# Kernel tuning notes

Measured on AMD Instinct MI355X. Metric: run time of the kernel, lower is better.

## Reference

```python
import jax, jax.numpy as jnp
import numpy as np

B, N, D, H = 8, 2048, 128, 4
DH = D // H
EPS_LN = 1e-5


def setup_inputs() -> dict:
    key = jax.random.key(0)
    ks = jax.random.split(key, 9)
    x = jax.random.normal(ks[0], (B, N, D), dtype=jnp.float32)
    u = jax.random.uniform(ks[1], (N, N), dtype=jnp.float32)
    adj = jnp.where(u > 0.5, u, 0.0)
    adj = adj.at[jnp.arange(N), jnp.arange(N)].set(1.0)
    W = jax.random.normal(ks[2], (D, D), dtype=jnp.float32) * (1.0 / np.sqrt(D))
    a_src = jax.random.normal(ks[3], (H, DH), dtype=jnp.float32) * 0.02
    a_dst = jax.random.normal(ks[4], (H, DH), dtype=jnp.float32) * 0.02
    Wo = jax.random.normal(ks[5], (D, D), dtype=jnp.float32) * (1.0 / np.sqrt(D))
    bo = jnp.zeros((D,), dtype=jnp.float32)
    gamma = jnp.ones((D,), dtype=jnp.float32)
    beta = jnp.zeros((D,), dtype=jnp.float32)
    return {"x": x, "adj_static": adj, "W": W, "a_src": a_src, "a_dst": a_dst,
            "Wo": Wo, "bo": bo, "gamma": gamma, "beta": beta}


def reference(x, adj_static, W, a_src, a_dst, Wo, bo, gamma, beta):
    # h: (B, H, N, DH)
    h = (x @ W.T).reshape(B, N, H, DH).transpose(0, 2, 1, 3)
    src = jnp.einsum('bhnd,hd->bhn', h, a_src)  # (B, H, N)
    dst = jnp.einsum('bhnd,hd->bhn', h, a_dst)  # (B, H, N)
    e = jax.nn.leaky_relu(src[..., :, None] + dst[..., None, :], 0.2)  # (B,H,N,N)
    logA = jnp.log(jnp.clip(adj_static, 1e-8))[None, None]
    mask = (adj_static > 0)[None, None]
    e = jnp.where(mask, e + logA, -jnp.inf)
    attn = jax.nn.softmax(e, axis=-1)  # dropout is identity in eval mode
    out = attn @ h  # (B, H, N, DH)
    out = out.transpose(0, 2, 1, 3).reshape(B, N, D)
    out = out @ Wo.T + bo
    y = x + out
    mu = jnp.mean(y, axis=-1, keepdims=True)
    var = jnp.mean(jnp.square(y - mu), axis=-1, keepdims=True)
    return (y - mu) * jax.lax.rsqrt(var + EPS_LN) * gamma + beta
```

## Files before the change

kernel.cpp:

```cpp
#include <hip/hip_runtime.h>

typedef short bf16x8 __attribute__((ext_vector_type(8)));
typedef float f32x4  __attribute__((ext_vector_type(4)));
typedef int   i32x4  __attribute__((ext_vector_type(4)));
typedef unsigned int u32x2 __attribute__((ext_vector_type(2)));

#define DEV static __device__ __forceinline__
#define LOG2E 1.4426950408889634f

DEV float bfu_to_f(unsigned short s) { return __builtin_bit_cast(float, (unsigned int)s << 16); }
DEV unsigned short f_to_bf(float f) {
  unsigned int u = __builtin_bit_cast(unsigned int, f);
  u += 0x7fffu + ((u >> 16) & 1u);
  return (unsigned short)(u >> 16);
}
DEV unsigned int pack_bf_rne(float lo, float hi) {
  return (unsigned int)f_to_bf(lo) | ((unsigned int)f_to_bf(hi) << 16);
}
DEV unsigned int pack_bf_rtz(float lo, float hi) {
#if __has_builtin(__builtin_amdgcn_perm)
  return __builtin_amdgcn_perm(__builtin_bit_cast(unsigned int, hi),
                               __builtin_bit_cast(unsigned int, lo), 0x07060302u);
#else
  return (__builtin_bit_cast(unsigned int, hi) & 0xffff0000u) |
         (__builtin_bit_cast(unsigned int, lo) >> 16);
#endif
}

DEV bool detect_f32(const void* adj) { return ((const float*)adj)[0] == 1.0f; }

template<bool F32> DEV float ldS(const void* p, size_t i) {
  if constexpr (F32) return ((const float*)p)[i];
  else               return bfu_to_f(((const unsigned short*)p)[i]);
}
template<bool F32> DEV void ld8f(const void* p, size_t i, float* o) {
  if constexpr (F32) {
    const float* f = (const float*)p + i;
    f32x4 a = *(const f32x4*)f, b = *(const f32x4*)(f + 4);
    o[0]=a[0]; o[1]=a[1]; o[2]=a[2]; o[3]=a[3];
    o[4]=b[0]; o[5]=b[1]; o[6]=b[2]; o[7]=b[3];
  } else {
    i32x4 w = *(const i32x4*)((const unsigned short*)p + i);
#pragma unroll
    for (int k = 0; k < 4; ++k) {
      unsigned int u = (unsigned int)w[k];
      o[2*k]   = __builtin_bit_cast(float, u << 16);
      o[2*k+1] = __builtin_bit_cast(float, u & 0xffff0000u);
    }
  }
}
template<bool F32> DEV bf16x8 ldfrag(const void* p, size_t i) {
  if constexpr (F32) {
    float o[8]; ld8f<true>(p, i, o);
    union { bf16x8 v; unsigned short u[8]; } r;
#pragma unroll
    for (int k = 0; k < 8; ++k) r.u[k] = f_to_bf(o[k]);
    return r.v;
  } else {
    return __builtin_bit_cast(bf16x8, *(const i32x4*)((const unsigned short*)p + i));
  }
}

template<bool F32> DEV void k_h_body(const void* __restrict__ x, const void* __restrict__ W,
                                     unsigned short* __restrict__ hT,
                                     unsigned short (&t_s)[16][136]) {
  const int tid = threadIdx.x, lane = tid & 63, wave = tid >> 6;
  const int nt = blockIdx.x >> 3, ct = blockIdx.x & 7;
  const int m = lane & 15, q = lane >> 4;
  bf16x8 wf[4];
#pragma unroll
  for (int k = 0; k < 4; ++k)
    wf[k] = ldfrag<F32>(W, (size_t)(ct * 16 + m) * 128 + q * 8 + k * 32);
#pragma unroll
  for (int s = 0; s < 2; ++s) {
    const int nsub = wave * 2 + s;
    const size_t xr = (size_t)(nt * 128 + nsub * 16 + m) * 128 + q * 8;
    f32x4 acc = {0.f, 0.f, 0.f, 0.f};
#pragma unroll
    for (int k = 0; k < 4; ++k)
      acc = __builtin_amdgcn_mfma_f32_16x16x32_bf16(ldfrag<F32>(x, xr + k * 32), wf[k],
                                                    acc, 0, 0, 0);
    u32x2 w2; w2[0] = pack_bf_rne(acc[0], acc[1]); w2[1] = pack_bf_rne(acc[2], acc[3]);
    *(u32x2*)&t_s[m][nsub * 16 + q * 4] = w2;
  }
  __syncthreads();
  const int row = tid >> 4, c8 = tid & 15;
  const int chg = ct * 16 + row, hh = chg >> 5, dloc = chg & 31;
  const int ng = nt * 128 + c8 * 8, b = ng >> 11, nl = ng & 2047;
  i32x4 v = *(const i32x4*)&t_s[row][c8 * 8];
  *(i32x4*)(hT + ((size_t)((b * 4 + hh) * 32 + dloc)) * 2048 + nl) = v;
}
__global__ __launch_bounds__(256) void k_h(const void* x, const void* W,
                                           unsigned short* hT, const void* adj) {
  __shared__ __align__(16) unsigned short t_s[16][136];
  if (detect_f32(adj)) k_h_body<true>(x, W, hT, t_s); else k_h_body<false>(x, W, hT, t_s);
}

template<bool F32> DEV void k_sd_body(const unsigned short* __restrict__ hT,
                                      const void* __restrict__ a_src, const void* __restrict__ a_dst,
                                      float* __restrict__ srcv, float* __restrict__ dstv) {
  const int t = blockIdx.x * 256 + threadIdx.x;
  const int n = t & 2047, bh = t >> 11, hh = bh & 3;
  const unsigned short* col = hT + (size_t)bh * 32 * 2048 + n;
  float s = 0.f, d = 0.f;
#pragma unroll
  for (int dd = 0; dd < 32; ++dd) {
    const float v = bfu_to_f(col[(size_t)dd * 2048]);
    s += v * ldS<F32>(a_src, hh * 32 + dd);
    d += v * ldS<F32>(a_dst, hh * 32 + dd);
  }
  srcv[t] = s * LOG2E; dstv[t] = d * LOG2E;
}
__global__ __launch_bounds__(256) void k_sd(const unsigned short* hT, const void* a_src,
                                            const void* a_dst, float* srcv, float* dstv,
                                            const void* adj) {
  if (detect_f32(adj)) k_sd_body<true>(hT, a_src, a_dst, srcv, dstv);
  else                 k_sd_body<false>(hT, a_src, a_dst, srcv, dstv);
}

struct SmemAttn {
  unsigned short adj[2][64][136];
  unsigned short vt[2][32][136];
  float dst[2048];
};

template<bool F32> DEV void k_attn_body(SmemAttn& sm, const void* __restrict__ adjv,
                                        const unsigned short* __restrict__ hT,
                                        const float* __restrict__ srcv,
                                        const float* __restrict__ dstv,
                                        unsigned short* __restrict__ ao) {
  const int tid = threadIdx.x, lane = tid & 63, wave = tid >> 6;
  const int bh = blockIdx.x & 31, i64 = blockIdx.x >> 5;
  const int b = bh >> 2, hh = bh & 3;
  const int m = lane & 15, q = lane >> 4;
  const int i0 = i64 * 64;
  const int il = wave * 16 + m;
  const int srow = tid >> 4, scol = (tid & 15) * 8;

  {
    const float* dp = dstv + bh * 2048 + tid * 8;
    *(f32x4*)&sm.dst[tid * 8]     = *(const f32x4*)dp;
    *(f32x4*)&sm.dst[tid * 8 + 4] = *(const f32x4*)(dp + 4);
  }

  f32x4 fr[8];
  i32x4 br[4];
  i32x4 vr[2];

#pragma unroll
  for (int p = 0; p < 4; ++p) {
    const size_t g = (size_t)(i0 + p * 16 + srow) * 2048 + scol;
    if constexpr (F32) {
      fr[2*p]   = *(const f32x4*)((const float*)adjv + g);
      fr[2*p+1] = *(const f32x4*)((const float*)adjv + g + 4);
    } else {
      br[p] = *(const i32x4*)((const unsigned short*)adjv + g);
    }
  }
#pragma unroll
  for (int p = 0; p < 2; ++p)
    vr[p] = *(const i32x4*)(hT + ((size_t)bh * 32 + p * 16 + srow) * 2048 + scol);
#pragma unroll
  for (int p = 0; p < 4; ++p) {
    i32x4 w;
    if constexpr (F32) {
      w[0] = (int)pack_bf_rtz(fr[2*p][0], fr[2*p][1]);
      w[1] = (int)pack_bf_rtz(fr[2*p][2], fr[2*p][3]);
      w[2] = (int)pack_bf_rtz(fr[2*p+1][0], fr[2*p+1][1]);
      w[3] = (int)pack_bf_rtz(fr[2*p+1][2], fr[2*p+1][3]);
    } else w = br[p];
    *(i32x4*)&sm.adj[0][p * 16 + srow][scol] = w;
  }
#pragma unroll
  for (int p = 0; p < 2; ++p) *(i32x4*)&sm.vt[0][p * 16 + srow][scol] = vr[p];
  __syncthreads();

  const float src_i = srcv[bh * 2048 + i0 + il];
  f32x4 acc0 = {0.f,0.f,0.f,0.f}, acc1 = {0.f,0.f,0.f,0.f};
  f32x4 acc2 = {0.f,0.f,0.f,0.f};
  i32x4 ones4;
  ones4[0] = ones4[1] = ones4[2] = ones4[3] = (int)0x3F803F80u;
  const bf16x8 Aones = __builtin_bit_cast(bf16x8, ones4);

  for (int c = 0; c < 16; ++c) {
    const int cb = c & 1;
    const bool pf = (c < 15);
    if (pf) {
      const int j1 = (c + 1) * 128;
#pragma unroll
      for (int p = 0; p < 4; ++p) {
        const size_t g = (size_t)(i0 + p * 16 + srow) * 2048 + j1 + scol;
        if constexpr (F32) {
          fr[2*p]   = *(const f32x4*)((const float*)adjv + g);
          fr[2*p+1] = *(const f32x4*)((const float*)adjv + g + 4);
        } else {
          br[p] = *(const i32x4*)((const unsigned short*)adjv + g);
        }
      }
#pragma unroll
      for (int p = 0; p < 2; ++p)
        vr[p] = *(const i32x4*)(hT + ((size_t)bh * 32 + p * 16 + srow) * 2048 + j1 + scol);
    }
#pragma unroll
    for (int jc = 0; jc < 4; ++jc) {
      const int jq = jc * 32 + q * 8;
      i32x4 aw = *(const i32x4*)&sm.adj[cb][il][jq];
      f32x4 d0 = *(const f32x4*)&sm.dst[c * 128 + jq];
      f32x4 d1 = *(const f32x4*)&sm.dst[c * 128 + jq + 4];
      bf16x8 A0 = *(const bf16x8*)&sm.vt[cb][m][jq];
      bf16x8 A1 = *(const bf16x8*)&sm.vt[cb][16 + m][jq];
      float a[8];
#pragma unroll
      for (int t = 0; t < 4; ++t) {
        unsigned int w = (unsigned int)aw[t];
        a[2*t]   = __builtin_bit_cast(float, w << 16);
        a[2*t+1] = __builtin_bit_cast(float, w & 0xffff0000u);
      }
      float p[8];
#pragma unroll
      for (int pp = 0; pp < 8; ++pp) {
        const float s = src_i + ((pp < 4) ? d0[pp] : d1[pp - 4]);
        const float l = fmaxf(s, 0.2f * s);
        p[pp] = a[pp] * exp2f(l);
      }
      i32x4 pk4;
      pk4[0] = (int)pack_bf_rtz(p[0], p[1]);
      pk4[1] = (int)pack_bf_rtz(p[2], p[3]);
      pk4[2] = (int)pack_bf_rtz(p[4], p[5]);
      pk4[3] = (int)pack_bf_rtz(p[6], p[7]);
      const bf16x8 pkv = __builtin_bit_cast(bf16x8, pk4);
      acc0 = __builtin_amdgcn_mfma_f32_16x16x32_bf16(A0, pkv, acc0, 0, 0, 0);
      acc1 = __builtin_amdgcn_mfma_f32_16x16x32_bf16(A1, pkv, acc1, 0, 0, 0);
      acc2 = __builtin_amdgcn_mfma_f32_16x16x32_bf16(Aones, pkv, acc2, 0, 0, 0);
    }
    if (pf) {
      const int nb = cb ^ 1;
#pragma unroll
      for (int p = 0; p < 4; ++p) {
        i32x4 w;
        if constexpr (F32) {
          w[0] = (int)pack_bf_rtz(fr[2*p][0], fr[2*p][1]);
          w[1] = (int)pack_bf_rtz(fr[2*p][2], fr[2*p][3]);
          w[2] = (int)pack_bf_rtz(fr[2*p+1][0], fr[2*p+1][1]);
          w[3] = (int)pack_bf_rtz(fr[2*p+1][2], fr[2*p+1][3]);
        } else w = br[p];
        *(i32x4*)&sm.adj[nb][p * 16 + srow][scol] = w;
      }
#pragma unroll
      for (int p = 0; p < 2; ++p) *(i32x4*)&sm.vt[nb][p * 16 + srow][scol] = vr[p];
    }
    __syncthreads();
  }

  const float inv = 1.f / fmaxf(acc2[0], 1e-20f);

  unsigned short* op = ao + ((size_t)(b * 2048) + i0 + il) * 128 + hh * 32 + q * 4;
  u32x2 w0, w1;
  w0[0] = pack_bf_rne(acc0[0] * inv, acc0[1] * inv);
  w0[1] = pack_bf_rne(acc0[2] * inv, acc0[3] * inv);
  w1[0] = pack_bf_rne(acc1[0] * inv, acc1[1] * inv);
  w1[1] = pack_bf_rne(acc1[2] * inv, acc1[3] * inv);
  *(u32x2*)op        = w0;
  *(u32x2*)(op + 16) = w1;
}
__global__ __launch_bounds__(256) void k_attn(const void* adj, const unsigned short* hT,
                                              const float* srcv, const float* dstv,
                                              unsigned short* ao) {
  __shared__ __align__(16) SmemAttn sm;
  if (detect_f32(adj)) k_attn_body<true>(sm, adj, hT, srcv, dstv, ao);
  else                 k_attn_body<false>(sm, adj, hT, srcv, dstv, ao);
}

template<bool F32> DEV void k_out_body(const unsigned short* __restrict__ ao,
                                       const void* __restrict__ Wo, const void* __restrict__ bo,
                                       const void* __restrict__ x, const void* __restrict__ gamma,
                                       const void* __restrict__ beta, void* __restrict__ out,
                                       float (&y_s)[16][132]) {
  const int tid = threadIdx.x, lane = tid & 63, wave = tid >> 6;
  const int m = lane & 15, q = lane >> 4;
  const int rbase = blockIdx.x * 16;
  bf16x8 af[4];
#pragma unroll
  for (int k = 0; k < 4; ++k)
    af[k] = ldfrag<false>(ao, ((size_t)(rbase + m)) * 128 + q * 8 + k * 32);
  f32x4 acc[2] = {{0.f,0.f,0.f,0.f},{0.f,0.f,0.f,0.f}};
#pragma unroll
  for (int ct = 0; ct < 2; ++ct) {
    const size_t wrow = (size_t)(wave * 32 + ct * 16 + m) * 128 + q * 8;
#pragma unroll
    for (int k = 0; k < 4; ++k)
      acc[ct] = __builtin_amdgcn_mfma_f32_16x16x32_bf16(af[k], ldfrag<F32>(Wo, wrow + k * 32),
                                                        acc[ct], 0, 0, 0);
  }
#pragma unroll
  for (int ct = 0; ct < 2; ++ct) {
    const int c = wave * 32 + ct * 16 + m;
    const float bov = ldS<F32>(bo, c);
#pragma unroll
    for (int r = 0; r < 4; ++r) {
      const int row = q * 4 + r;
      y_s[row][c] = acc[ct][r] + bov + ldS<F32>(x, (size_t)(rbase + row) * 128 + c);
    }
  }
  __syncthreads();
  const int r = tid >> 4, c16 = tid & 15;
  float vals[8], sum = 0.f, sq = 0.f;
#pragma unroll
  for (int k = 0; k < 8; ++k) {
    const float v = y_s[r][c16 * 8 + k];
    vals[k] = v; sum += v; sq += v * v;
  }
#pragma unroll
  for (int msk = 1; msk < 16; msk <<= 1) {
    sum += __shfl_xor(sum, msk, 16);
    sq  += __shfl_xor(sq,  msk, 16);
  }
  const float mu  = sum * (1.f / 128.f);
  const float var = fmaxf(sq * (1.f / 128.f) - mu * mu, 0.f);
  const float rstd = rsqrtf(var + 1e-5f);
  float o[8];
#pragma unroll
  for (int k = 0; k < 8; ++k) {
    const int c = c16 * 8 + k;
    o[k] = (vals[k] - mu) * rstd * ldS<F32>(gamma, c) + ldS<F32>(beta, c);
  }
  const size_t obase = (size_t)(rbase + r) * 128 + c16 * 8;
  if constexpr (F32) {
    float* op = (float*)out + obase;
    f32x4 w0 = {o[0],o[1],o[2],o[3]}, w1 = {o[4],o[5],o[6],o[7]};
    *(f32x4*)op = w0; *(f32x4*)(op + 4) = w1;
  } else {
    union { unsigned short u[8]; i32x4 v; } ob;
#pragma unroll
    for (int k = 0; k < 8; ++k) ob.u[k] = f_to_bf(o[k]);
    *(i32x4*)((unsigned short*)out + obase) = ob.v;
  }
}
__global__ __launch_bounds__(256) void k_out(const unsigned short* ao, const void* Wo,
                                             const void* bo, const void* x, const void* gamma,
                                             const void* beta, void* out, const void* adj) {
  __shared__ __align__(16) float y_s[16][132];
  if (detect_f32(adj)) k_out_body<true>(ao, Wo, bo, x, gamma, beta, out, y_s);
  else                 k_out_body<false>(ao, Wo, bo, x, gamma, beta, out, y_s);
}

extern "C" void kernel_launch(void* const* d_in, const int* in_sizes, int n_in,
                              void* d_out, int out_size, void* d_ws, size_t ws_size,
                              hipStream_t stream) {
  const void* x     = d_in[0];
  const void* adj   = d_in[1];
  const void* W     = d_in[2];
  const void* a_src = d_in[3];
  const void* a_dst = d_in[4];
  const void* Wo    = d_in[5];
  const void* bo    = d_in[6];
  const void* gamma = d_in[7];
  const void* beta  = d_in[8];

  char* ws = (char*)d_ws;
  unsigned short* hT_ws  = (unsigned short*)ws;
  unsigned short* ao_ws  = (unsigned short*)(ws + 4194304);
  float*          src_ws = (float*)(ws + 8388608);
  float*          dst_ws = (float*)(ws + 8650752);

  k_h   <<<1024, 256, 0, stream>>>(x, W, hT_ws, adj);
  k_sd  <<<256,  256, 0, stream>>>(hT_ws, a_src, a_dst, src_ws, dst_ws, adj);
  k_attn<<<1024, 256, 0, stream>>>(adj, hT_ws, src_ws, dst_ws, ao_ws);
  k_out <<<1024, 256, 0, stream>>>(ao_ws, Wo, bo, x, gamma, beta, d_out, adj);
}
```

Baseline: 175.8 us.

## Share adjacency tile across two heads per 512-thread attention block

Each attention block now handles two (batch,head) pairs with 512 threads, so every adjacency tile loaded into shared memory serves both heads. This halves global adjacency traffic and the fp32-to-bf16 conversion work. The dst vector is now streamed per chunk with double buffering rather than preloaded whole, and row padding changes from 136 to 132. The risks are bank conflicts from the new padding, fewer blocks in the grid, and register pressure under the new launch bounds.

```diff
diff --git a/kernel.cpp b/kernel.cpp
--- a/kernel.cpp
+++ b/kernel.cpp
@@ -119,9 +119,9 @@
 }
 
 struct SmemAttn {
-  unsigned short adj[2][64][136];
-  unsigned short vt[2][32][136];
-  float dst[2048];
+  unsigned short adj[2][64][132];
+  unsigned short vt[2][2][32][132];
+  float dst[2][2][128];
 };
 
 template<bool F32> DEV void k_attn_body(SmemAttn& sm, const void* __restrict__ adjv,
@@ -130,49 +130,46 @@
                                         const float* __restrict__ dstv,
                                         unsigned short* __restrict__ ao) {
   const int tid = threadIdx.x, lane = tid & 63, wave = tid >> 6;
-  const int bh = blockIdx.x & 31, i64 = blockIdx.x >> 5;
+  const int bhp = blockIdx.x & 15, i64 = blockIdx.x >> 4;
+  const int sub = wave >> 2, w4 = wave & 3;
+  const int bh = bhp * 2 + sub;
   const int b = bh >> 2, hh = bh & 3;
   const int m = lane & 15, q = lane >> 4;
   const int i0 = i64 * 64;
-  const int il = wave * 16 + m;
-  const int srow = tid >> 4, scol = (tid & 15) * 8;
+  const int il = w4 * 16 + m;
+
+  const int arow = tid >> 3, acol = (tid & 7) * 16;
+  const int vsub = tid >> 8, vd = (tid >> 3) & 31, vcol = (tid & 7) * 16;
+  const bool dstg = (tid & 7) == 0;
+  const int dk = tid >> 3, dsub = dk >> 5, dj = (dk & 31) * 4;
+
+  f32x4 fr[4];
+  i32x4 br[2];
+  i32x4 vr[2];
+  f32x4 dr;
 
   {
-    const float* dp = dstv + bh * 2048 + tid * 8;
-    *(f32x4*)&sm.dst[tid * 8]     = *(const f32x4*)dp;
-    *(f32x4*)&sm.dst[tid * 8 + 4] = *(const f32x4*)(dp + 4);
-  }
-
-  f32x4 fr[8];
-  i32x4 br[4];
-  i32x4 vr[2];
-
-#pragma unroll
-  for (int p = 0; p < 4; ++p) {
-    const size_t g = (size_t)(i0 + p * 16 + srow) * 2048 + scol;
+    const size_t ga = (size_t)(i0 + arow) * 2048 + acol;
+    i32x4 w0, w1;
     if constexpr (F32) {
-      fr[2*p]   = *(const f32x4*)((const float*)adjv + g);
-      fr[2*p+1] = *(const f32x4*)((const float*)adjv + g + 4);
+#pragma unroll
+      for (int p = 0; p < 4; ++p) fr[p] = *(const f32x4*)((const float*)adjv + ga + p * 4);
+      w0[0]=(int)pack_bf_rtz(fr[0][0],fr[0][1]); w0[1]=(int)pack_bf_rtz(fr[0][2],fr[0][3]);
+      w0[2]=(int)pack_bf_rtz(fr[1][0],fr[1][1]); w0[3]=(int)pack_bf_rtz(fr[1][2],fr[1][3]);
+      w1[0]=(int)pack_bf_rtz(fr[2][0],fr[2][1]); w1[1]=(int)pack_bf_rtz(fr[2][2],fr[2][3]);
+      w1[2]=(int)pack_bf_rtz(fr[3][0],fr[3][1]); w1[3]=(int)pack_bf_rtz(fr[3][2],fr[3][3]);
     } else {
-      br[p] = *(const i32x4*)((const unsigned short*)adjv + g);
-    }
-  }
-#pragma unroll
-  for (int p = 0; p < 2; ++p)
-    vr[p] = *(const i32x4*)(hT + ((size_t)bh * 32 + p * 16 + srow) * 2048 + scol);
-#pragma unroll
-  for (int p = 0; p < 4; ++p) {
-    i32x4 w;
-    if constexpr (F32) {
-      w[0] = (int)pack_bf_rtz(fr[2*p][0], fr[2*p][1]);
-      w[1] = (int)pack_bf_rtz(fr[2*p][2], fr[2*p][3]);
-      w[2] = (int)pack_bf_rtz(fr[2*p+1][0], fr[2*p+1][1]);
-      w[3] = (int)pack_bf_rtz(fr[2*p+1][2], fr[2*p+1][3]);
-    } else w = br[p];
-    *(i32x4*)&sm.adj[0][p * 16 + srow][scol] = w;
-  }
-#pragma unroll
-  for (int p = 0; p < 2; ++p) *(i32x4*)&sm.vt[0][p * 16 + srow][scol] = vr[p];
+      w0 = *(const i32x4*)((const unsigned short*)adjv + ga);
+      w1 = *(const i32x4*)((const unsigned short*)adjv + ga + 8);
+    }
+    *(i32x4*)&sm.adj[0][arow][acol]     = w0;
+    *(i32x4*)&sm.adj[0][arow][acol + 8] = w1;
+    const unsigned short* vp = hT + ((size_t)((bhp * 2 + vsub) * 32 + vd)) * 2048 + vcol;
+    *(i32x4*)&sm.vt[0][vsub][vd][vcol]     = *(const i32x4*)vp;
+    *(i32x4*)&sm.vt[0][vsub][vd][vcol + 8] = *(const i32x4*)(vp + 8);
+    if (dstg)
+      *(f32x4*)&sm.dst[0][dsub][dj] = *(const f32x4*)(dstv + (size_t)(bhp * 2 + dsub) * 2048 + dj);
+  }
   __syncthreads();
 
   const float src_i = srcv[bh * 2048 + i0 + il];
@@ -187,28 +184,28 @@
     const bool pf = (c < 15);
     if (pf) {
       const int j1 = (c + 1) * 128;
-#pragma unroll
-      for (int p = 0; p < 4; ++p) {
-        const size_t g = (size_t)(i0 + p * 16 + srow) * 2048 + j1 + scol;
-        if constexpr (F32) {
-          fr[2*p]   = *(const f32x4*)((const float*)adjv + g);
-          fr[2*p+1] = *(const f32x4*)((const float*)adjv + g + 4);
-        } else {
-          br[p] = *(const i32x4*)((const unsigned short*)adjv + g);
-        }
+      const size_t ga = (size_t)(i0 + arow) * 2048 + j1 + acol;
+      if constexpr (F32) {
+#pragma unroll
+        for (int p = 0; p < 4; ++p) fr[p] = *(const f32x4*)((const float*)adjv + ga + p * 4);
+      } else {
+        br[0] = *(const i32x4*)((const unsigned short*)adjv + ga);
+        br[1] = *(const i32x4*)((const unsigned short*)adjv + ga + 8);
       }
-#pragma unroll
-      for (int p = 0; p < 2; ++p)
-        vr[p] = *(const i32x4*)(hT + ((size_t)bh * 32 + p * 16 + srow) * 2048 + j1 + scol);
+      const unsigned short* vp = hT + ((size_t)((bhp * 2 + vsub) * 32 + vd)) * 2048 + j1 + vcol;
+      vr[0] = *(const i32x4*)vp;
+      vr[1] = *(const i32x4*)(vp + 8);
+      if (dstg)
+        dr = *(const f32x4*)(dstv + (size_t)(bhp * 2 + dsub) * 2048 + j1 + dj);
     }
 #pragma unroll
     for (int jc = 0; jc < 4; ++jc) {
       const int jq = jc * 32 + q * 8;
       i32x4 aw = *(const i32x4*)&sm.adj[cb][il][jq];
-      f32x4 d0 = *(const f32x4*)&sm.dst[c * 128 + jq];
-      f32x4 d1 = *(const f32x4*)&sm.dst[c * 128 + jq + 4];
-      bf16x8 A0 = *(const bf16x8*)&sm.vt[cb][m][jq];
-      bf16x8 A1 = *(const bf16x8*)&sm.vt[cb][16 + m][jq];
+      f32x4 d0 = *(const f32x4*)&sm.dst[cb][sub][jq];
+      f32x4 d1 = *(const f32x4*)&sm.dst[cb][sub][jq + 4];
+      bf16x8 A0 = *(const bf16x8*)&sm.vt[cb][sub][m][jq];
+      bf16x8 A1 = *(const bf16x8*)&sm.vt[cb][sub][16 + m][jq];
       float a[8];
 #pragma unroll
       for (int t = 0; t < 4; ++t) {
@@ -235,19 +232,18 @@
     }
     if (pf) {
       const int nb = cb ^ 1;
-#pragma unroll
-      for (int p = 0; p < 4; ++p) {
-        i32x4 w;
-        if constexpr (F32) {
-          w[0] = (int)pack_bf_rtz(fr[2*p][0], fr[2*p][1]);
-          w[1] = (int)pack_bf_rtz(fr[2*p][2], fr[2*p][3]);
-          w[2] = (int)pack_bf_rtz(fr[2*p+1][0], fr[2*p+1][1]);
-          w[3] = (int)pack_bf_rtz(fr[2*p+1][2], fr[2*p+1][3]);
-        } else w = br[p];
-        *(i32x4*)&sm.adj[nb][p * 16 + srow][scol] = w;
-      }
-#pragma unroll
-      for (int p = 0; p < 2; ++p) *(i32x4*)&sm.vt[nb][p * 16 + srow][scol] = vr[p];
+      i32x4 w0, w1;
+      if constexpr (F32) {
+        w0[0]=(int)pack_bf_rtz(fr[0][0],fr[0][1]); w0[1]=(int)pack_bf_rtz(fr[0][2],fr[0][3]);
+        w0[2]=(int)pack_bf_rtz(fr[1][0],fr[1][1]); w0[3]=(int)pack_bf_rtz(fr[1][2],fr[1][3]);
+        w1[0]=(int)pack_bf_rtz(fr[2][0],fr[2][1]); w1[1]=(int)pack_bf_rtz(fr[2][2],fr[2][3]);
+        w1[2]=(int)pack_bf_rtz(fr[3][0],fr[3][1]); w1[3]=(int)pack_bf_rtz(fr[3][2],fr[3][3]);
+      } else { w0 = br[0]; w1 = br[1]; }
+      *(i32x4*)&sm.adj[nb][arow][acol]     = w0;
+      *(i32x4*)&sm.adj[nb][arow][acol + 8] = w1;
+      *(i32x4*)&sm.vt[nb][vsub][vd][vcol]     = vr[0];
+      *(i32x4*)&sm.vt[nb][vsub][vd][vcol + 8] = vr[1];
+      if (dstg) *(f32x4*)&sm.dst[nb][dsub][dj] = dr;
     }
     __syncthreads();
   }
@@ -263,9 +259,9 @@
   *(u32x2*)op        = w0;
   *(u32x2*)(op + 16) = w1;
 }
-__global__ __launch_bounds__(256) void k_attn(const void* adj, const unsigned short* hT,
-                                              const float* srcv, const float* dstv,
-                                              unsigned short* ao) {
+__global__ __launch_bounds__(512, 4) void k_attn(const void* adj, const unsigned short* hT,
+                                                 const float* srcv, const float* dstv,
+                                                 unsigned short* ao) {
   __shared__ __align__(16) SmemAttn sm;
   if (detect_f32(adj)) k_attn_body<true>(sm, adj, hT, srcv, dstv, ao);
   else                 k_attn_body<false>(sm, adj, hT, srcv, dstv, ao);
@@ -365,6 +361,6 @@
 
   k_h   <<<1024, 256, 0, stream>>>(x, W, hT_ws, adj);
   k_sd  <<<256,  256, 0, stream>>>(hT_ws, a_src, a_dst, src_ws, dst_ws, adj);
-  k_attn<<<1024, 256, 0, stream>>>(adj, hT_ws, src_ws, dst_ws, ao_ws);
+  k_attn<<<512,  512, 0, stream>>>(adj, hT_ws, src_ws, dst_ws, ao_ws);
   k_out <<<1024, 256, 0, stream>>>(ao_ws, Wo, bo, x, gamma, beta, d_out, adj);
 }
```

After: 174.6 us. About the same (-0.7%).
